# Kernel optimization log

Measured on AMD Instinct MI355X. Metric: run time of the kernel, lower is better.

## Reference

```python
import jax, jax.numpy as jnp
import numpy as np

SIZE = (160, 192, 224)  # (D, H, W)


def setup_inputs() -> dict:
    key = jax.random.key(0)
    k1, k2 = jax.random.split(key)
    src = jax.random.normal(k1, (2, 1) + SIZE, dtype=jnp.float32)
    flow = jax.random.normal(k2, (2, 3) + SIZE, dtype=jnp.float32)
    return {"src": src, "flow": flow}


def _warp3d(src, flow):
    # src: [B, C, D, H, W]; flow: [B, 3, D, H, W] (voxel displacements, (d,h,w) order)
    # Equivalent to: normalize (grid+flow) to [-1,1], permute/flip, then
    # F.grid_sample(align_corners=True, mode='bilinear', padding_mode='zeros').
    # The normalization and grid_sample's un-normalization cancel exactly, so we
    # sample src at voxel coords grid+flow with trilinear interp, zeros padding.
    B, C, D, H, W = src.shape
    dt = src.dtype
    gd, gh, gw = jnp.meshgrid(
        jnp.arange(D, dtype=dt), jnp.arange(H, dtype=dt), jnp.arange(W, dtype=dt),
        indexing="ij")
    cd = gd[None] + flow[:, 0]  # [B, D, H, W]
    ch = gh[None] + flow[:, 1]
    cw = gw[None] + flow[:, 2]

    d0f = jnp.floor(cd); h0f = jnp.floor(ch); w0f = jnp.floor(cw)
    fd = cd - d0f; fh = ch - h0f; fw = cw - w0f  # fractional weights
    d0 = d0f.astype(jnp.int32); h0 = h0f.astype(jnp.int32); w0 = w0f.astype(jnp.int32)

    src_flat = src.reshape(B, C, D * H * W)
    out = jnp.zeros((B, C, D, H, W), dt)
    for dd in (0, 1):
        wd = fd if dd else (1.0 - fd)
        idd = d0 + dd
        for hh in (0, 1):
            wh = fh if hh else (1.0 - fh)
            ihh = h0 + hh
            for ww in (0, 1):
                wwt = fw if ww else (1.0 - fw)
                iww = w0 + ww
                valid = ((idd >= 0) & (idd < D) & (ihh >= 0) & (ihh < H)
                         & (iww >= 0) & (iww < W)).astype(dt)
                lin = ((jnp.clip(idd, 0, D - 1) * H + jnp.clip(ihh, 0, H - 1)) * W
                       + jnp.clip(iww, 0, W - 1))  # [B, D, H, W]
                vals = jnp.take_along_axis(
                    src_flat, lin.reshape(B, 1, -1), axis=2).reshape(B, C, D, H, W)
                out = out + vals * (wd * wh * wwt * valid)[:, None]
    return out


def reference(src, flow):
    return _warp3d(src, flow)
```

## Files before the change

kernel.cpp:

```cpp
#include <hip/hip_runtime.h>


#define DD 160
#define HH 192
#define WW 224
constexpr int DHW = DD * HH * WW;
constexpr int BLOCK = 512;
constexpr int DT = DD / 16;
constexpr int HT = HH / 8;
constexpr int WT = WW / 16;
constexpr int BRICKS_PER_B = DT * HT * WT;
constexpr int NWG = 2 * BRICKS_PER_B;
constexpr int NXCD = 8;
constexpr int CHUNK = NWG / NXCD;

constexpr int RD = 24, RH = 16, RWE = 24, RWP = 25;
constexpr int TILE_N = RD * RH * RWP;
constexpr int SROWS = RD * RH;
constexpr int SCHUNKS = SROWS * 6;

typedef float vfloat4 __attribute__((ext_vector_type(4)));

__device__ __forceinline__ float trilerp_global(const float* __restrict__ sbase,
                                                float cd, float ch, float cw) {
    float d0f = floorf(cd), h0f = floorf(ch), w0f = floorf(cw);
    float fd = cd - d0f, fh = ch - h0f, fw = cw - w0f;
    int d0 = (int)d0f, h0 = (int)h0f, w0 = (int)w0f;
    int d1 = d0 + 1, h1 = h0 + 1, w1 = w0 + 1;

    float wd0 = (1.0f - fd) * ((unsigned)d0 < (unsigned)DD ? 1.0f : 0.0f);
    float wd1 = fd          * ((unsigned)d1 < (unsigned)DD ? 1.0f : 0.0f);
    float wh0 = (1.0f - fh) * ((unsigned)h0 < (unsigned)HH ? 1.0f : 0.0f);
    float wh1 = fh          * ((unsigned)h1 < (unsigned)HH ? 1.0f : 0.0f);
    float ww0 = (1.0f - fw) * ((unsigned)w0 < (unsigned)WW ? 1.0f : 0.0f);
    float ww1 = fw          * ((unsigned)w1 < (unsigned)WW ? 1.0f : 0.0f);

    int d0c = min(max(d0, 0), DD - 1), d1c = min(max(d1, 0), DD - 1);
    int h0c = min(max(h0, 0), HH - 1), h1c = min(max(h1, 0), HH - 1);
    int w0c = min(max(w0, 0), WW - 1), w1c = min(max(w1, 0), WW - 1);

    const float* p00 = sbase + (d0c * HH + h0c) * WW;
    const float* p01 = sbase + (d0c * HH + h1c) * WW;
    const float* p10 = sbase + (d1c * HH + h0c) * WW;
    const float* p11 = sbase + (d1c * HH + h1c) * WW;

    return wd0 * (wh0 * (ww0 * p00[w0c] + ww1 * p00[w1c]) +
                  wh1 * (ww0 * p01[w0c] + ww1 * p01[w1c])) +
           wd1 * (wh0 * (ww0 * p10[w0c] + ww1 * p10[w1c]) +
                  wh1 * (ww0 * p11[w0c] + ww1 * p11[w1c]));
}

__global__ __launch_bounds__(512, 8) void warp3d_kernel(
    const float* __restrict__ src, const float* __restrict__ flow,
    float* __restrict__ out) {
    __shared__ float tile[TILE_N];

    int bid = blockIdx.x;
    int wg  = (bid & 7) * CHUNK + (bid >> 3);

    int b  = wg / BRICKS_PER_B;
    int r  = wg - b * BRICKS_PER_B;
    int dt = r / (HT * WT);
    int r2 = r - dt * (HT * WT);
    int ht = r2 / WT;
    int wtile = r2 - ht * WT;

    int dB = dt * 16, hB = ht * 8, wB = wtile * 16;
    int dB4 = dB - 4, hB4 = hB - 4, wB4 = wB - 4;

    bool interior = (dt >= 1) & (dt <= DT - 2) & (ht >= 1) & (ht <= HT - 2)
                  & (wtile >= 1) & (wtile <= WT - 2);

    const float* sbase = src + (size_t)b * DHW;

    int tid  = threadIdx.x;
    int wave = tid >> 6;
    int lane = tid & 63;
    int d = dB + (wave >> 1) * 4 + (lane >> 4);
    int h = hB + (wave & 1) * 4 + ((lane >> 2) & 3);
    int w = wB + (lane & 3) * 4;

    size_t sOff = (size_t)(d * HH + h) * WW + w;
    const float* fb = flow + (size_t)b * 3 * DHW + sOff;
    vfloat4 fld = *reinterpret_cast<const vfloat4*>(fb);
    vfloat4 flh = *reinterpret_cast<const vfloat4*>(fb + DHW);
    vfloat4 flw = *reinterpret_cast<const vfloat4*>(fb + 2 * DHW);

    bool wedge = (wtile == 0) | (wtile == WT - 1);
    for (int u = tid; u < SCHUNKS; u += BLOCK) {
        int row = u / 6;
        int c   = u - row * 6;
        int ld = row >> 4, lh = row & 15;
        int dg = min(max(dB4 + ld, 0), DD - 1);
        int hg = min(max(hB4 + lh, 0), HH - 1);
        const float* grow = sbase + (size_t)(dg * HH + hg) * WW;
        int wg0 = wB4 + 4 * c;
        vfloat4 v;
        if (!wedge) {
            v = *reinterpret_cast<const vfloat4*>(grow + wg0);
        } else {
            v.x = grow[min(max(wg0 + 0, 0), WW - 1)];
            v.y = grow[min(max(wg0 + 1, 0), WW - 1)];
            v.z = grow[min(max(wg0 + 2, 0), WW - 1)];
            v.w = grow[min(max(wg0 + 3, 0), WW - 1)];
        }
        float* dst = &tile[row * RWP + 4 * c];
        dst[0] = v.x; dst[1] = v.y; dst[2] = v.z; dst[3] = v.w;
    }
    __syncthreads();

    float df = (float)d, hf = (float)h, wf = (float)w;
    float fdv[4] = {fld.x, fld.y, fld.z, fld.w};
    float fhv[4] = {flh.x, flh.y, flh.z, flh.w};
    float fwv[4] = {flw.x, flw.y, flw.z, flw.w};

    float cdv[4], chv[4], cwv[4];
    float fdq[4], fhq[4], fwq[4];
    int   base[4];
    bool  okv[4];
    #pragma unroll
    for (int k = 0; k < 4; ++k) {
        float cd = df + fdv[k], ch = hf + fhv[k], cw = wf + (float)k + fwv[k];
        cdv[k] = cd; chv[k] = ch; cwv[k] = cw;
        float d0f = floorf(cd), h0f = floorf(ch), w0f = floorf(cw);
        fdq[k] = cd - d0f; fhq[k] = ch - h0f; fwq[k] = cw - w0f;
        int rd = (int)d0f - dB4, rh = (int)h0f - hB4, rw = (int)w0f - wB4;
        okv[k] = ((unsigned)rd < (unsigned)(RD - 1)) &
                 ((unsigned)rh < (unsigned)(RH - 1)) &
                 ((unsigned)rw < (unsigned)(RWE - 1));
        base[k] = (rd * RH + rh) * RWP + rw;
    }
    bool allin = okv[0] & okv[1] & okv[2] & okv[3];

    float res[4];
    if (allin) {
        if (interior) {
            #pragma unroll
            for (int k = 0; k < 4; ++k) {
                int b0 = base[k];
                float fw = fwq[k], fh = fhq[k], fd = fdq[k];
                float v0 = tile[b0],                 v1 = tile[b0 + 1];
                float v2 = tile[b0 + RWP],           v3 = tile[b0 + RWP + 1];
                float v4 = tile[b0 + RH * RWP],      v5 = tile[b0 + RH * RWP + 1];
                float v6 = tile[b0 + RH * RWP + RWP];
                float v7 = tile[b0 + RH * RWP + RWP + 1];
                float x0 = fmaf(fw, v1 - v0, v0);
                float x1 = fmaf(fw, v3 - v2, v2);
                float x2 = fmaf(fw, v5 - v4, v4);
                float x3 = fmaf(fw, v7 - v6, v6);
                float y0 = fmaf(fh, x1 - x0, x0);
                float y1 = fmaf(fh, x3 - x2, x2);
                res[k] = fmaf(fd, y1 - y0, y0);
            }
        } else {
            #pragma unroll
            for (int k = 0; k < 4; ++k) {
                float cd = cdv[k], ch = chv[k], cw = cwv[k];
                int d0 = (int)floorf(cd), h0 = (int)floorf(ch),
                    w0 = (int)floorf(cw);
                float fd = fdq[k], fh = fhq[k], fw = fwq[k];
                float wd0 = (1.0f - fd) * ((unsigned)d0 < (unsigned)DD ? 1.0f : 0.0f);
                float wd1 = fd    * ((unsigned)(d0 + 1) < (unsigned)DD ? 1.0f : 0.0f);
                float wh0 = (1.0f - fh) * ((unsigned)h0 < (unsigned)HH ? 1.0f : 0.0f);
                float wh1 = fh    * ((unsigned)(h0 + 1) < (unsigned)HH ? 1.0f : 0.0f);
                float ww0 = (1.0f - fw) * ((unsigned)w0 < (unsigned)WW ? 1.0f : 0.0f);
                float ww1 = fw    * ((unsigned)(w0 + 1) < (unsigned)WW ? 1.0f : 0.0f);
                int b0 = base[k];
                float v0 = tile[b0],                 v1 = tile[b0 + 1];
                float v2 = tile[b0 + RWP],           v3 = tile[b0 + RWP + 1];
                float v4 = tile[b0 + RH * RWP],      v5 = tile[b0 + RH * RWP + 1];
                float v6 = tile[b0 + RH * RWP + RWP];
                float v7 = tile[b0 + RH * RWP + RWP + 1];
                float a = wd0 * wh0, bq = wd0 * wh1, cq = wd1 * wh0, dq = wd1 * wh1;
                res[k] = a  * (ww0 * v0 + ww1 * v1) + bq * (ww0 * v2 + ww1 * v3) +
                         cq * (ww0 * v4 + ww1 * v5) + dq * (ww0 * v6 + ww1 * v7);
            }
        }
    } else {
        #pragma unroll
        for (int k = 0; k < 4; ++k)
            res[k] = trilerp_global(sbase, cdv[k], chv[k], cwv[k]);
    }

    vfloat4 o4 = {res[0], res[1], res[2], res[3]};
    *reinterpret_cast<vfloat4*>(out + (size_t)b * DHW + sOff) = o4;
}

extern "C" void kernel_launch(void* const* d_in, const int* in_sizes, int n_in,
                              void* d_out, int out_size, void* d_ws, size_t ws_size,
                              hipStream_t stream) {
    const float* src  = (const float*)d_in[0];
    const float* flow = (const float*)d_in[1];
    float* out = (float*)d_out;

    warp3d_kernel<<<NWG, BLOCK, 0, stream>>>(src, flow, out);
}
```

Before: 69.46 us.

## Store LDS tile as packed bf16 neighbor pairs to halve LDS reads

The shared-memory tile now holds, for each position, a 32-bit word packing the rounded bf16 values of that voxel and its w+1 neighbor. Each trilinear sample therefore needs 4 LDS reads instead of 8. The padded row width shrinks from 25 to 23, and staging does one extra global load per chunk. The cost is precision: src values are rounded to bf16 on the fast paths, which may break tolerance and changes the LDS bank-conflict pattern.

```diff
diff --git a/kernel.cpp b/kernel.cpp
--- a/kernel.cpp
+++ b/kernel.cpp
@@ -14,12 +14,25 @@
 constexpr int NXCD = 8;
 constexpr int CHUNK = NWG / NXCD;
 
-constexpr int RD = 24, RH = 16, RWE = 24, RWP = 25;
-constexpr int TILE_N = RD * RH * RWP;
+constexpr int RD = 24, RH = 16, RWE = 24;
+constexpr int PW = 23;
 constexpr int SROWS = RD * RH;
-constexpr int SCHUNKS = SROWS * 6;
+constexpr int TILE_N = SROWS * PW;
+constexpr int DROW = RH * PW;
 
 typedef float vfloat4 __attribute__((ext_vector_type(4)));
+
+__device__ __forceinline__ unsigned packpair(float a, float b) {
+    unsigned ua = __float_as_uint(a) + 0x8000u;
+    unsigned ub = __float_as_uint(b) + 0x8000u;
+    return (ua >> 16) | (ub & 0xFFFF0000u);
+}
+__device__ __forceinline__ float plo(unsigned u) {
+    return __uint_as_float(u << 16);
+}
+__device__ __forceinline__ float phi(unsigned u) {
+    return __uint_as_float(u & 0xFFFF0000u);
+}
 
 __device__ __forceinline__ float trilerp_global(const float* __restrict__ sbase,
                                                 float cd, float ch, float cw) {
@@ -53,7 +66,7 @@
 __global__ __launch_bounds__(512, 8) void warp3d_kernel(
     const float* __restrict__ src, const float* __restrict__ flow,
     float* __restrict__ out) {
-    __shared__ float tile[TILE_N];
+    __shared__ unsigned tile[TILE_N];
 
     int bid = blockIdx.x;
     int wg  = (bid & 7) * CHUNK + (bid >> 3);
@@ -87,7 +100,7 @@
     vfloat4 flw = *reinterpret_cast<const vfloat4*>(fb + 2 * DHW);
 
     bool wedge = (wtile == 0) | (wtile == WT - 1);
-    for (int u = tid; u < SCHUNKS; u += BLOCK) {
+    for (int u = tid; u < SROWS * 6; u += BLOCK) {
         int row = u / 6;
         int c   = u - row * 6;
         int ld = row >> 4, lh = row & 15;
@@ -95,17 +108,23 @@
         int hg = min(max(hB4 + lh, 0), HH - 1);
         const float* grow = sbase + (size_t)(dg * HH + hg) * WW;
         int wg0 = wB4 + 4 * c;
-        vfloat4 v;
+        float v0, v1, v2, v3, v4;
         if (!wedge) {
-            v = *reinterpret_cast<const vfloat4*>(grow + wg0);
+            vfloat4 q = *reinterpret_cast<const vfloat4*>(grow + wg0);
+            v0 = q.x; v1 = q.y; v2 = q.z; v3 = q.w;
+            v4 = (c < 5) ? grow[wg0 + 4] : 0.0f;
         } else {
-            v.x = grow[min(max(wg0 + 0, 0), WW - 1)];
-            v.y = grow[min(max(wg0 + 1, 0), WW - 1)];
-            v.z = grow[min(max(wg0 + 2, 0), WW - 1)];
-            v.w = grow[min(max(wg0 + 3, 0), WW - 1)];
+            v0 = grow[min(max(wg0 + 0, 0), WW - 1)];
+            v1 = grow[min(max(wg0 + 1, 0), WW - 1)];
+            v2 = grow[min(max(wg0 + 2, 0), WW - 1)];
+            v3 = grow[min(max(wg0 + 3, 0), WW - 1)];
+            v4 = grow[min(max(wg0 + 4, 0), WW - 1)];
         }
-        float* dst = &tile[row * RWP + 4 * c];
-        dst[0] = v.x; dst[1] = v.y; dst[2] = v.z; dst[3] = v.w;
+        unsigned* dst = &tile[row * PW + 4 * c];
+        dst[0] = packpair(v0, v1);
+        dst[1] = packpair(v1, v2);
+        dst[2] = packpair(v2, v3);
+        if (c < 5) dst[3] = packpair(v3, v4);
     }
     __syncthreads();
 
@@ -128,7 +147,7 @@
         okv[k] = ((unsigned)rd < (unsigned)(RD - 1)) &
                  ((unsigned)rh < (unsigned)(RH - 1)) &
                  ((unsigned)rw < (unsigned)(RWE - 1));
-        base[k] = (rd * RH + rh) * RWP + rw;
+        base[k] = (rd * RH + rh) * PW + rw;
     }
     bool allin = okv[0] & okv[1] & okv[2] & okv[3];
 
@@ -139,15 +158,18 @@
             for (int k = 0; k < 4; ++k) {
                 int b0 = base[k];
                 float fw = fwq[k], fh = fhq[k], fd = fdq[k];
-                float v0 = tile[b0],                 v1 = tile[b0 + 1];
-                float v2 = tile[b0 + RWP],           v3 = tile[b0 + RWP + 1];
-                float v4 = tile[b0 + RH * RWP],      v5 = tile[b0 + RH * RWP + 1];
-                float v6 = tile[b0 + RH * RWP + RWP];
-                float v7 = tile[b0 + RH * RWP + RWP + 1];
-                float x0 = fmaf(fw, v1 - v0, v0);
-                float x1 = fmaf(fw, v3 - v2, v2);
-                float x2 = fmaf(fw, v5 - v4, v4);
-                float x3 = fmaf(fw, v7 - v6, v6);
+                unsigned u0 = tile[b0];
+                unsigned u1 = tile[b0 + PW];
+                unsigned u2 = tile[b0 + DROW];
+                unsigned u3 = tile[b0 + DROW + PW];
+                float a0 = plo(u0), a1 = phi(u0);
+                float b1 = plo(u1), b2 = phi(u1);
+                float c0 = plo(u2), c1 = phi(u2);
+                float e0 = plo(u3), e1 = phi(u3);
+                float x0 = fmaf(fw, a1 - a0, a0);
+                float x1 = fmaf(fw, b2 - b1, b1);
+                float x2 = fmaf(fw, c1 - c0, c0);
+                float x3 = fmaf(fw, e1 - e0, e0);
                 float y0 = fmaf(fh, x1 - x0, x0);
                 float y1 = fmaf(fh, x3 - x2, x2);
                 res[k] = fmaf(fd, y1 - y0, y0);
@@ -155,9 +177,8 @@
         } else {
             #pragma unroll
             for (int k = 0; k < 4; ++k) {
-                float cd = cdv[k], ch = chv[k], cw = cwv[k];
-                int d0 = (int)floorf(cd), h0 = (int)floorf(ch),
-                    w0 = (int)floorf(cw);
+                int d0 = (int)floorf(cdv[k]), h0 = (int)floorf(chv[k]),
+                    w0 = (int)floorf(cwv[k]);
                 float fd = fdq[k], fh = fhq[k], fw = fwq[k];
                 float wd0 = (1.0f - fd) * ((unsigned)d0 < (unsigned)DD ? 1.0f : 0.0f);
                 float wd1 = fd    * ((unsigned)(d0 + 1) < (unsigned)DD ? 1.0f : 0.0f);
@@ -166,14 +187,15 @@
                 float ww0 = (1.0f - fw) * ((unsigned)w0 < (unsigned)WW ? 1.0f : 0.0f);
                 float ww1 = fw    * ((unsigned)(w0 + 1) < (unsigned)WW ? 1.0f : 0.0f);
                 int b0 = base[k];
-                float v0 = tile[b0],                 v1 = tile[b0 + 1];
-                float v2 = tile[b0 + RWP],           v3 = tile[b0 + RWP + 1];
-                float v4 = tile[b0 + RH * RWP],      v5 = tile[b0 + RH * RWP + 1];
-                float v6 = tile[b0 + RH * RWP + RWP];
-                float v7 = tile[b0 + RH * RWP + RWP + 1];
+                unsigned u0 = tile[b0];
+                unsigned u1 = tile[b0 + PW];
+                unsigned u2 = tile[b0 + DROW];
+                unsigned u3 = tile[b0 + DROW + PW];
                 float a = wd0 * wh0, bq = wd0 * wh1, cq = wd1 * wh0, dq = wd1 * wh1;
-                res[k] = a  * (ww0 * v0 + ww1 * v1) + bq * (ww0 * v2 + ww1 * v3) +
-                         cq * (ww0 * v4 + ww1 * v5) + dq * (ww0 * v6 + ww1 * v7);
+                res[k] = a  * (ww0 * plo(u0) + ww1 * phi(u0)) +
+                         bq * (ww0 * plo(u1) + ww1 * phi(u1)) +
+                         cq * (ww0 * plo(u2) + ww1 * phi(u2)) +
+                         dq * (ww0 * plo(u3) + ww1 * phi(u3));
             }
         }
     } else {
```

Result: slower. 87.31 us (+25.7%).

## Load source halo tile directly into LDS via global_load_lds and defer barrier

Applied to the files above, without the earlier changes.

Replaces the register-staged vec4 halo copy with direct global-to-LDS 16-byte loads (global_load_lds) for non-edge bricks. The tile row stride changes from 25 to 24 so each wave's contiguous chunks map linearly into LDS. The barrier moves after the coordinate and flow math so that work overlaps the async fills, and the coordinate arrays are recomputed instead of kept live to save registers. Removing the padding may add LDS bank conflicts in the trilinear gathers. The async-load path also depends on the barrier providing the needed wait for the LDS writes to complete.

```diff
diff --git a/kernel.cpp b/kernel.cpp
--- a/kernel.cpp
+++ b/kernel.cpp
@@ -14,10 +14,12 @@
 constexpr int NXCD = 8;
 constexpr int CHUNK = NWG / NXCD;
 
-constexpr int RD = 24, RH = 16, RWE = 24, RWP = 25;
-constexpr int TILE_N = RD * RH * RWP;
+constexpr int RD = 24, RH = 16, RWE = 24, RWS = 24;
+constexpr int TILE_N = RD * RH * RWS;
 constexpr int SROWS = RD * RH;
 constexpr int SCHUNKS = SROWS * 6;
+constexpr int WCHUNKS = SCHUNKS / 8;
+constexpr int DROW = RH * RWS;
 
 typedef float vfloat4 __attribute__((ext_vector_type(4)));
 
@@ -53,7 +55,7 @@
 __global__ __launch_bounds__(512, 8) void warp3d_kernel(
     const float* __restrict__ src, const float* __restrict__ flow,
     float* __restrict__ out) {
-    __shared__ float tile[TILE_N];
+    __shared__ __align__(16) float tile[TILE_N];
 
     int bid = blockIdx.x;
     int wg  = (bid & 7) * CHUNK + (bid >> 3);
@@ -87,50 +89,66 @@
     vfloat4 flw = *reinterpret_cast<const vfloat4*>(fb + 2 * DHW);
 
     bool wedge = (wtile == 0) | (wtile == WT - 1);
-    for (int u = tid; u < SCHUNKS; u += BLOCK) {
-        int row = u / 6;
-        int c   = u - row * 6;
-        int ld = row >> 4, lh = row & 15;
-        int dg = min(max(dB4 + ld, 0), DD - 1);
-        int hg = min(max(hB4 + lh, 0), HH - 1);
-        const float* grow = sbase + (size_t)(dg * HH + hg) * WW;
-        int wg0 = wB4 + 4 * c;
-        vfloat4 v;
-        if (!wedge) {
-            v = *reinterpret_cast<const vfloat4*>(grow + wg0);
-        } else {
+    if (!wedge) {
+        int wbase = wave * WCHUNKS;
+        #pragma unroll
+        for (int it = 0; it < 5; ++it) {
+            int u = wbase + it * 64 + lane;
+            if (u < SCHUNKS) {
+                int row = u / 6;
+                int c   = u - row * 6;
+                int ld = row >> 4, lh = row & 15;
+                int dg = min(max(dB4 + ld, 0), DD - 1);
+                int hg = min(max(hB4 + lh, 0), HH - 1);
+                const float* gsrc = sbase + (size_t)(dg * HH + hg) * WW
+                                  + (wB4 + 4 * c);
+                __builtin_amdgcn_global_load_lds(
+                    (const __attribute__((address_space(1))) unsigned int*)gsrc,
+                    (__attribute__((address_space(3))) unsigned int*)
+                        &tile[(size_t)(wbase + it * 64) * 4],
+                    16, 0, 0);
+            }
+        }
+    } else {
+        for (int u = tid; u < SCHUNKS; u += BLOCK) {
+            int row = u / 6;
+            int c   = u - row * 6;
+            int ld = row >> 4, lh = row & 15;
+            int dg = min(max(dB4 + ld, 0), DD - 1);
+            int hg = min(max(hB4 + lh, 0), HH - 1);
+            const float* grow = sbase + (size_t)(dg * HH + hg) * WW;
+            int wg0 = wB4 + 4 * c;
+            vfloat4 v;
             v.x = grow[min(max(wg0 + 0, 0), WW - 1)];
             v.y = grow[min(max(wg0 + 1, 0), WW - 1)];
             v.z = grow[min(max(wg0 + 2, 0), WW - 1)];
             v.w = grow[min(max(wg0 + 3, 0), WW - 1)];
+            *reinterpret_cast<vfloat4*>(&tile[u * 4]) = v;
         }
-        float* dst = &tile[row * RWP + 4 * c];
-        dst[0] = v.x; dst[1] = v.y; dst[2] = v.z; dst[3] = v.w;
     }
-    __syncthreads();
 
     float df = (float)d, hf = (float)h, wf = (float)w;
     float fdv[4] = {fld.x, fld.y, fld.z, fld.w};
     float fhv[4] = {flh.x, flh.y, flh.z, flh.w};
     float fwv[4] = {flw.x, flw.y, flw.z, flw.w};
 
-    float cdv[4], chv[4], cwv[4];
     float fdq[4], fhq[4], fwq[4];
     int   base[4];
     bool  okv[4];
     #pragma unroll
     for (int k = 0; k < 4; ++k) {
         float cd = df + fdv[k], ch = hf + fhv[k], cw = wf + (float)k + fwv[k];
-        cdv[k] = cd; chv[k] = ch; cwv[k] = cw;
         float d0f = floorf(cd), h0f = floorf(ch), w0f = floorf(cw);
         fdq[k] = cd - d0f; fhq[k] = ch - h0f; fwq[k] = cw - w0f;
         int rd = (int)d0f - dB4, rh = (int)h0f - hB4, rw = (int)w0f - wB4;
         okv[k] = ((unsigned)rd < (unsigned)(RD - 1)) &
                  ((unsigned)rh < (unsigned)(RH - 1)) &
                  ((unsigned)rw < (unsigned)(RWE - 1));
-        base[k] = (rd * RH + rh) * RWP + rw;
+        base[k] = (rd * RH + rh) * RWS + rw;
     }
     bool allin = okv[0] & okv[1] & okv[2] & okv[3];
+
+    __syncthreads();
 
     float res[4];
     if (allin) {
@@ -140,10 +158,10 @@
                 int b0 = base[k];
                 float fw = fwq[k], fh = fhq[k], fd = fdq[k];
                 float v0 = tile[b0],                 v1 = tile[b0 + 1];
-                float v2 = tile[b0 + RWP],           v3 = tile[b0 + RWP + 1];
-                float v4 = tile[b0 + RH * RWP],      v5 = tile[b0 + RH * RWP + 1];
-                float v6 = tile[b0 + RH * RWP + RWP];
-                float v7 = tile[b0 + RH * RWP + RWP + 1];
+                float v2 = tile[b0 + RWS],           v3 = tile[b0 + RWS + 1];
+                float v4 = tile[b0 + DROW],          v5 = tile[b0 + DROW + 1];
+                float v6 = tile[b0 + DROW + RWS];
+                float v7 = tile[b0 + DROW + RWS + 1];
                 float x0 = fmaf(fw, v1 - v0, v0);
                 float x1 = fmaf(fw, v3 - v2, v2);
                 float x2 = fmaf(fw, v5 - v4, v4);
@@ -155,7 +173,8 @@
         } else {
             #pragma unroll
             for (int k = 0; k < 4; ++k) {
-                float cd = cdv[k], ch = chv[k], cw = cwv[k];
+                float cd = df + fdv[k], ch = hf + fhv[k],
+                      cw = wf + (float)k + fwv[k];
                 int d0 = (int)floorf(cd), h0 = (int)floorf(ch),
                     w0 = (int)floorf(cw);
                 float fd = fdq[k], fh = fhq[k], fw = fwq[k];
@@ -167,10 +186,10 @@
                 float ww1 = fw    * ((unsigned)(w0 + 1) < (unsigned)WW ? 1.0f : 0.0f);
                 int b0 = base[k];
                 float v0 = tile[b0],                 v1 = tile[b0 + 1];
-                float v2 = tile[b0 + RWP],           v3 = tile[b0 + RWP + 1];
-                float v4 = tile[b0 + RH * RWP],      v5 = tile[b0 + RH * RWP + 1];
-                float v6 = tile[b0 + RH * RWP + RWP];
-                float v7 = tile[b0 + RH * RWP + RWP + 1];
+                float v2 = tile[b0 + RWS],           v3 = tile[b0 + RWS + 1];
+                float v4 = tile[b0 + DROW],          v5 = tile[b0 + DROW + 1];
+                float v6 = tile[b0 + DROW + RWS];
+                float v7 = tile[b0 + DROW + RWS + 1];
                 float a = wd0 * wh0, bq = wd0 * wh1, cq = wd1 * wh0, dq = wd1 * wh1;
                 res[k] = a  * (ww0 * v0 + ww1 * v1) + bq * (ww0 * v2 + ww1 * v3) +
                          cq * (ww0 * v4 + ww1 * v5) + dq * (ww0 * v6 + ww1 * v7);
@@ -179,7 +198,8 @@
     } else {
         #pragma unroll
         for (int k = 0; k < 4; ++k)
-            res[k] = trilerp_global(sbase, cdv[k], chv[k], cwv[k]);
+            res[k] = trilerp_global(sbase, df + fdv[k], hf + fhv[k],
+                                    wf + (float)k + fwv[k]);
     }
 
     vfloat4 o4 = {res[0], res[1], res[2], res[3]};
```

Result: slower. 75.46 us (+8.6%).
